# Optimization experiments

Hardware: AMD Instinct MI355X
Metric: run time of the kernel (lower is better)

Reference implementation:

```python
import jax, jax.numpy as jnp
import numpy as np

C1, C2, C3, S = 3, 6, 3, 16
SPLITS = (9 * C1 * 1, C1, 9 * C2 * C1, C2, 9 * C3 * C2, C3, 9 * S * C3, S)  # sums to 811
B = 16384


def _channelize(w, cin, cout):
    # w: [B, cout*9*cin] -> filter [3, 3, cin, B*cout] (B-major on out axis)
    w = w.reshape(-1, cout, 9 * cin)
    w = jnp.transpose(w, (2, 0, 1))          # [9*cin, B, cout]
    return w.reshape(3, 3, cin, -1)


def _gconv(x, w, groups):
    # x: [1, H, W, B*cin], w: [3, 3, cin, B*cout]; grouped conv, groups=B
    return jax.lax.conv_general_dilated(
        x, w, window_strides=(1, 1), padding='VALID',
        dimension_numbers=('NHWC', 'HWIO', 'NHWC'),
        feature_group_count=groups)


def _maxpool2(x):
    return jax.lax.reduce_window(x, -jnp.inf, jax.lax.max,
                                 (1, 2, 2, 1), (1, 2, 2, 1), 'VALID')


def setup_inputs() -> dict:
    key = jax.random.key(0)
    ks = jax.random.split(key, 8)
    tot = sum(SPLITS)
    return {
        'image': jax.random.normal(ks[0], (1, 28, 28, B), jnp.float32),
        'state': jax.random.normal(ks[1], (B, S), jnp.float32),
        'W1': jax.random.normal(ks[2], (S, 16), jnp.float32) * 0.25,
        'b1': jnp.zeros((16,), jnp.float32),
        'W2': jax.random.normal(ks[3], (16, 16), jnp.float32) * 0.25,
        'b2': jnp.zeros((16,), jnp.float32),
        'W3': jax.random.normal(ks[4], (16, tot), jnp.float32) * 0.1,
        'b3': jnp.zeros((tot,), jnp.float32),
    }


def reference(image, state, W1, b1, W2, b2, W3, b3):
    batch = state.shape[0]
    # Hypernetwork MLP producing per-sample conv weights (dropout rate 0 => identity)
    h = jax.nn.relu(state @ W1 + b1)
    h = jax.nn.relu(h @ W2 + b2)
    w = h @ W3 + b3                               # [B, 811]
    idx = np.cumsum(SPLITS)[:-1]
    w1, bb1, w2, bb2, w3, bb3, w4, bb4 = jnp.split(w, idx, axis=1)

    x = _gconv(image, _channelize(w1, 1, C1), batch) + bb1.reshape(-1)   # [1,26,26,B*C1]
    x = _maxpool2(jax.nn.relu(x))                                        # [1,13,13,B*C1]
    x = _gconv(x, _channelize(w2, C1, C2), batch) + bb2.reshape(-1)      # [1,11,11,B*C2]
    x = _maxpool2(jax.nn.relu(x))                                        # [1,5,5,B*C2]
    x = _gconv(x, _channelize(w3, C2, C3), batch) + bb3.reshape(-1)      # [1,3,3,B*C3]
    x = jax.nn.relu(x)
    x = _gconv(x, _channelize(w4, C3, S), batch) + bb4.reshape(-1)       # [1,1,1,B*S]
    x = jnp.transpose(x, (3, 1, 2, 0)).reshape(-1, S)                    # [B, S]
    return state + x
```

## Files before the change

### kernel.cpp

```cpp
#include <hip/hip_runtime.h>

#define BLK   512
#define NSAMP 8
#define REG   1480
#define OFF_P2   0
#define OFF_P3   152
#define OFF_W    392
#define HW_P1    2408
#define DW_P1    1204


typedef short bf16x8 __attribute__((ext_vector_type(8)));
typedef float f32x4  __attribute__((ext_vector_type(4)));
typedef float f32x2  __attribute__((ext_vector_type(2)));


__device__ __forceinline__ float bf2f(unsigned short u) {
    return __uint_as_float(((unsigned int)u) << 16);
}
__device__ __forceinline__ unsigned short f2bf(float f) {
    unsigned int x = __float_as_uint(f);
    return (unsigned short)((x + 0x7fffu + ((x >> 16) & 1u)) >> 16);
}
__device__ __forceinline__ void wsync() {
    __builtin_amdgcn_wave_barrier();
    __asm__ volatile("s_waitcnt lgkmcnt(0)" ::: "memory");
    __builtin_amdgcn_wave_barrier();
}

__device__ __forceinline__ bool is_bf16(const void* p, int elems) {
    const unsigned short* h = (const unsigned short*)p;
    int n = elems; if (n > 32) n = 32;
    int nz = 0, ok = 0;
    for (int i = 0; i < n; i += 2) {
        unsigned short u = h[i];
        if (u == 0) continue;
        ++nz;
        unsigned int e = (u >> 7) & 255u;
        if (e >= 100u && e <= 141u) ++ok;
    }
    if (nz < 4) return true;
    return 4 * ok >= 3 * nz;
}

__device__ __forceinline__ int wperm(int j) {
    if (j >= 30 && j < 192) {
        int rel = j - 30, c = rel / 27, r2 = rel - 27 * c;
        int tap = r2 / 3, ci = r2 - 3 * tap;
        return 30 + c * 27 + ci * 9 + tap;
    }
    if (j >= 198 && j < 360) {
        int rel = j - 198, c = rel / 54, r3 = rel - 54 * c;
        int tap = r3 / 6, ci = r3 - 6 * tap;
        return 198 + c * 54 + ci * 9 + tap;
    }
    return j;
}

__global__ __launch_bounds__(BLK, 4)
void dyncnn4_kernel(const void* __restrict__ image,
                    const void* __restrict__ state,
                    const void* __restrict__ W1, const void* __restrict__ b1,
                    const void* __restrict__ W2, const void* __restrict__ b2,
                    const void* __restrict__ W3, const void* __restrict__ b3,
                    void* __restrict__ out,
                    int B, int nswz)
{
    __shared__ float SH[NSAMP * REG];
    __shared__ float s_st[NSAMP][16];
    __shared__ float s_h1[NSAMP][16];
    __shared__ float s_h2[NSAMP][16];
    __shared__ unsigned char s_fl[8];
    __shared__ unsigned short s_pj[812];

    const int t    = threadIdx.x;
    const int wv   = t >> 6;
    const int lane = t & 63;
    const int hn   = lane & 15;
    const int kg   = lane >> 4;

    if (t < 8) {
        const void* q; int n;
        switch (t) {
            case 0:  q = image; n = 784 * B; break;
            case 1:  q = state; n = 16 * B;  break;
            case 2:  q = W1;    n = 256;     break;
            case 3:  q = b1;    n = 16;      break;
            case 4:  q = W2;    n = 256;     break;
            case 5:  q = b2;    n = 16;      break;
            case 6:  q = W3;    n = 12976;   break;
            default: q = b3;    n = 811;     break;
        }
        s_fl[t] = is_bf16(q, n) ? 1 : 0;
    }
    for (int j = t; j < 811; j += BLK)
        s_pj[j] = (unsigned short)wperm(j);
    __syncthreads();
    const bool im_bf = s_fl[0], st_bf = s_fl[1], w1_bf = s_fl[2], b1_bf = s_fl[3];
    const bool w2_bf = s_fl[4], b2_bf = s_fl[5], w3_bf = s_fl[6], b3_bf = s_fl[7];
    const bool out_bf = im_bf && st_bf && w1_bf && w2_bf && w3_bf;

    int p = blockIdx.x;
    int l = (nswz > 0) ? ((p & 7) * nswz + (p >> 3)) : p;
    const int b0 = l * NSAMP;

    unsigned short* su = (unsigned short*)SH;

    bf16x8 bp0 = {0,0,0,0,0,0,0,0}, bp1 = {0,0,0,0,0,0,0,0}, bp2 = {0,0,0,0,0,0,0,0},
           bp3 = {0,0,0,0,0,0,0,0}, bp4 = {0,0,0,0,0,0,0,0}, bp5 = {0,0,0,0,0,0,0,0},
           bp6 = {0,0,0,0,0,0,0,0};
    if (w3_bf) {
        const unsigned short* W3h = (const unsigned short*)W3;
#define PREF(T, BP) { const int tl = wv + (T) * 8; const int jn = tl * 16 + hn;      \
        if (kg < 2 && tl < 51 && jn < 811) {                                          \
            const unsigned short* q = W3h + (kg * 8) * 811 + jn;                      \
            BP[0] = (short)q[0];      BP[1] = (short)q[811];                          \
            BP[2] = (short)q[1622];   BP[3] = (short)q[2433];                         \
            BP[4] = (short)q[3244];   BP[5] = (short)q[4055];                         \
            BP[6] = (short)q[4866];   BP[7] = (short)q[5677]; } }
        PREF(0, bp0) PREF(1, bp1) PREF(2, bp2) PREF(3, bp3)
        PREF(4, bp4) PREF(5, bp5) PREF(6, bp6)
#undef PREF
    }

    if (wv < 2) {
        int s = wv * 4 + (lane >> 4), j = lane & 15;
        int gi = (b0 + s) * 16 + j;
        s_st[s][j] = st_bf ? bf2f(((const unsigned short*)state)[gi])
                           : ((const float*)state)[gi];
        wsync();
        float acc = b1_bf ? bf2f(((const unsigned short*)b1)[j])
                          : ((const float*)b1)[j];
#pragma unroll
        for (int k = 0; k < 16; ++k) {
            float w = w1_bf ? bf2f(((const unsigned short*)W1)[k * 16 + j])
                            : ((const float*)W1)[k * 16 + j];
            acc += s_st[s][k] * w;
        }
        s_h1[s][j] = fmaxf(acc, 0.f);
        wsync();
        acc = b2_bf ? bf2f(((const unsigned short*)b2)[j])
                    : ((const float*)b2)[j];
#pragma unroll
        for (int k = 0; k < 16; ++k) {
            float w = w2_bf ? bf2f(((const unsigned short*)W2)[k * 16 + j])
                            : ((const float*)W2)[k * 16 + j];
            acc += s_h1[s][k] * w;
        }
        s_h2[s][j] = fmaxf(acc, 0.f);
    } else {
        if (im_bf) {
            const unsigned short* im = (const unsigned short*)image;
            unsigned* sd = (unsigned*)SH;
            int d = t - 128;
            {
                const uint4 v0 = *(const uint4*)(im + (2 * d)     * B + b0);
                const uint4 v1 = *(const uint4*)(im + (2 * d + 1) * B + b0);
                unsigned a0[4] = {v0.x, v0.y, v0.z, v0.w};
                unsigned a1[4] = {v1.x, v1.y, v1.z, v1.w};
#pragma unroll
                for (int s = 0; s < 8; ++s) {
                    unsigned m = __builtin_amdgcn_perm(
                        a1[s >> 1], a0[s >> 1],
                        (s & 1) ? 0x07060302u : 0x05040100u);
                    sd[s * REG + d] = m;
                }
            }
            if (d < 8) {
                const int d2 = d + 384;
                const uint4 v0 = *(const uint4*)(im + (2 * d2)     * B + b0);
                const uint4 v1 = *(const uint4*)(im + (2 * d2 + 1) * B + b0);
                unsigned a0[4] = {v0.x, v0.y, v0.z, v0.w};
                unsigned a1[4] = {v1.x, v1.y, v1.z, v1.w};
#pragma unroll
                for (int s = 0; s < 8; ++s) {
                    unsigned m = __builtin_amdgcn_perm(
                        a1[s >> 1], a0[s >> 1],
                        (s & 1) ? 0x07060302u : 0x05040100u);
                    sd[s * REG + d2] = m;
                }
            }
        } else {
            const float* im = (const float*)image;
            int pix0 = t - 128;
            for (int pix = pix0; pix < 784; pix += 384) {
                const float4 a = *(const float4*)(im + pix * B + b0);
                const float4 c = *(const float4*)(im + pix * B + b0 + 4);
                su[0 * 2 * REG + pix] = f2bf(a.x);
                su[1 * 2 * REG + pix] = f2bf(a.y);
                su[2 * 2 * REG + pix] = f2bf(a.z);
                su[3 * 2 * REG + pix] = f2bf(a.w);
                su[4 * 2 * REG + pix] = f2bf(c.x);
                su[5 * 2 * REG + pix] = f2bf(c.y);
                su[6 * 2 * REG + pix] = f2bf(c.z);
                su[7 * 2 * REG + pix] = f2bf(c.w);
            }
        }
    }
    __syncthreads();

    {
        bf16x8 afrag;
#pragma unroll
        for (int i = 0; i < 8; ++i) afrag[i] = 0;
        if (kg < 2 && hn < 8) {
            const int k0 = kg * 8;
#pragma unroll
            for (int i = 0; i < 8; ++i)
                afrag[i] = (short)f2bf(s_h2[hn][k0 + i]);
        }
        const unsigned short* b3h = (const unsigned short*)b3;
        const float*          b3f = (const float*)b3;
        if (w3_bf) {
#define HTILE(T, BP) { const int tl = wv + (T) * 8; const int jn = tl * 16 + hn;     \
            f32x4 c = {0.f, 0.f, 0.f, 0.f};                                           \
            c = __builtin_amdgcn_mfma_f32_16x16x32_bf16(afrag, BP, c, 0, 0, 0);       \
            const int row0 = kg * 4;                                                  \
            if (tl < 51 && row0 < 8 && jn < 811) {                                    \
                float bb = b3_bf ? bf2f(b3h[jn]) : b3f[jn];                            \
                const int pj = (int)s_pj[jn];                                         \
                SH[(row0 + 0) * REG + OFF_W + pj] = c[0] + bb;                        \
                SH[(row0 + 1) * REG + OFF_W + pj] = c[1] + bb;                        \
                SH[(row0 + 2) * REG + OFF_W + pj] = c[2] + bb;                        \
                SH[(row0 + 3) * REG + OFF_W + pj] = c[3] + bb; } }
            HTILE(0, bp0) HTILE(1, bp1) HTILE(2, bp2) HTILE(3, bp3)
            HTILE(4, bp4) HTILE(5, bp5) HTILE(6, bp6)
#undef HTILE
        } else {
            for (int tile = wv; tile < 51; tile += 8) {
                const int jn = tile * 16 + hn;
                bf16x8 bfrag;
#pragma unroll
                for (int i = 0; i < 8; ++i) bfrag[i] = 0;
                if (kg < 2 && jn < 811) {
                    const int k0 = kg * 8;
                    const float* q = (const float*)W3 + k0 * 811 + jn;
#pragma unroll
                    for (int i = 0; i < 8; ++i) bfrag[i] = (short)f2bf(q[i * 811]);
                }
                f32x4 c = {0.f, 0.f, 0.f, 0.f};
                c = __builtin_amdgcn_mfma_f32_16x16x32_bf16(afrag, bfrag, c, 0, 0, 0);
                const int row0 = kg * 4;
                if (row0 < 8 && jn < 811) {
                    float bb = b3_bf ? bf2f(b3h[jn]) : b3f[jn];
                    const int pj = (int)s_pj[jn];
#pragma unroll
                    for (int r = 0; r < 4; ++r)
                        SH[(row0 + r) * REG + OFF_W + pj] = c[r] + bb;
                }
            }
        }
    }
    __syncthreads();

    const int sb  = wv * REG;
    const int sb2 = wv * 2 * REG;

    {
        float wc[27], cb[3];
#pragma unroll
        for (int i = 0; i < 27; ++i) wc[i] = SH[sb + OFF_W + i];
#pragma unroll
        for (int c = 0; c < 3; ++c) cb[c] = SH[sb + OFF_W + 27 + c];
        const unsigned* suw = (const unsigned*)&SH[sb];
#pragma unroll
        for (int it = 0; it < 3; ++it) {
            int pix = lane + it * 64;
            if (pix < 169) {
                int py = pix / 13, px = pix - py * 13;
                int iy = 2 * py;
                f32x2 P[4][3];
#pragma unroll
                for (int dy = 0; dy < 4; ++dy) {
                    int r = (iy + dy) * 14 + px;
                    unsigned d0 = suw[r], d1 = suw[r + 1];
                    float c0 = __uint_as_float(d0 << 16);
                    float c1 = __uint_as_float(d0 & 0xffff0000u);
                    float c2 = __uint_as_float(d1 << 16);
                    float c3 = __uint_as_float(d1 & 0xffff0000u);
                    P[dy][0] = (f32x2){c0, c1};
                    P[dy][1] = (f32x2){c1, c2};
                    P[dy][2] = (f32x2){c2, c3};
                }
                unsigned short* op = &su[sb2 + HW_P1 + py * 14 + px];
#pragma unroll
                for (int c = 0; c < 3; ++c) {
                    f32x2 at = {0.f, 0.f}, ab = {0.f, 0.f};
#pragma unroll
                    for (int ky = 0; ky < 3; ++ky)
#pragma unroll
                        for (int kx = 0; kx < 3; ++kx) {
                            float w = wc[c * 9 + ky * 3 + kx];
                            f32x2 ws = {w, w};
                            at += P[ky][kx]     * ws;
                            ab += P[ky + 1][kx] * ws;
                        }
                    float m = fmaxf(fmaxf(at.x, at.y), fmaxf(ab.x, ab.y));
                    op[c * 182] = f2bf(fmaxf(m + cb[c], 0.f));
                }
            }
        }
    }
    wsync();

    {
        int g = lane >> 5, q = lane & 31;
        if (q < 25) {
            int py = q / 5, px = q - py * 5;
            const unsigned* p1w = (const unsigned*)&SH[sb + DW_P1];
            f32x2 aT0 = {0.f, 0.f}, aB0 = {0.f, 0.f};
            f32x2 aT1 = {0.f, 0.f}, aB1 = {0.f, 0.f};
            f32x2 aT2 = {0.f, 0.f}, aB2 = {0.f, 0.f};
#pragma unroll
            for (int ci = 0; ci < 3; ++ci) {
                f32x2 P[4][3];
#pragma unroll
                for (int dy = 0; dy < 4; ++dy) {
                    int r = ci * 91 + (2 * py + dy) * 7 + px;
                    unsigned d0 = p1w[r], d1 = p1w[r + 1];
                    float c0 = __uint_as_float(d0 << 16);
                    float c1 = __uint_as_float(d0 & 0xffff0000u);
                    float c2 = __uint_as_float(d1 << 16);
                    float c3 = __uint_as_float(d1 & 0xffff0000u);
                    P[dy][0] = (f32x2){c0, c1};
                    P[dy][1] = (f32x2){c1, c2};
                    P[dy][2] = (f32x2){c2, c3};
                }
#pragma unroll
                for (int it = 0; it < 3; ++it) {
                    int c = it * 2 + g;
                    const int wo = sb + OFF_W + 30 + c * 27 + ci * 9;
#pragma unroll
                    for (int ky = 0; ky < 3; ++ky)
#pragma unroll
                        for (int kx = 0; kx < 3; ++kx) {
                            float w = SH[wo + ky * 3 + kx];
                            f32x2 ws = {w, w};
                            if (it == 0) { aT0 += P[ky][kx] * ws; aB0 += P[ky + 1][kx] * ws; }
                            if (it == 1) { aT1 += P[ky][kx] * ws; aB1 += P[ky + 1][kx] * ws; }
                            if (it == 2) { aT2 += P[ky][kx] * ws; aB2 += P[ky + 1][kx] * ws; }
                        }
                }
            }
#pragma unroll
            for (int it = 0; it < 3; ++it) {
                int c = it * 2 + g;
                f32x2 aT = (it == 0) ? aT0 : (it == 1) ? aT1 : aT2;
                f32x2 aB = (it == 0) ? aB0 : (it == 1) ? aB1 : aB2;
                float m = fmaxf(fmaxf(aT.x, aT.y), fmaxf(aB.x, aB.y));
                SH[sb + OFF_P2 + c * 25 + q] =
                    fmaxf(m + SH[sb + OFF_W + 192 + c], 0.f);
            }
        }
    }
    wsync();

    {
        float acc = 0.f;
        int pq = lane % 27;
        int half = lane / 27;
        int c = pq / 9, pos = pq - c * 9;
        int py = pos / 3, px = pos - py * 3;
        if (lane < 54) {
            const int cb3 = half * 3;
#pragma unroll
            for (int ci3 = 0; ci3 < 3; ++ci3) {
                const int ci = cb3 + ci3;
                const int wo = sb + OFF_W + 198 + c * 54 + ci * 9;
                float wr[9];
#pragma unroll
                for (int i = 0; i < 9; ++i) wr[i] = SH[wo + i];
                const int pbase = sb + OFF_P2 + ci * 25 + py * 5 + px;
#pragma unroll
                for (int ky = 0; ky < 3; ++ky)
#pragma unroll
                    for (int kx = 0; kx < 3; ++kx)
                        acc += SH[pbase + ky * 5 + kx] * wr[ky * 3 + kx];
            }
        }
        float other = __shfl(acc, (lane + 27) & 63);
        if (lane < 27)
            SH[sb + OFF_P3 + pos * 3 + c] =
                fmaxf(acc + other + SH[sb + OFF_W + 360 + c], 0.f);
    }
    wsync();

    {
        float acc = 0.f;
        int os = lane & 15, h = (lane >> 4) & 1;
        if (lane < 32) {
            const int wo = sb + OFF_W + 363 + os * 27;
            int p0 = h ? 4 : 0, p1 = h ? 9 : 4;
            for (int pp = p0; pp < p1; ++pp)
#pragma unroll
                for (int ci = 0; ci < 3; ++ci)
                    acc += SH[sb + OFF_P3 + pp * 3 + ci] * SH[wo + pp * 3 + ci];
        }
        float other = __shfl(acc, (lane + 16) & 63);
        if (lane < 16) {
            float tot = acc + other + SH[sb + OFF_W + 795 + os] + s_st[wv][os];
            int gi = (b0 + wv) * 16 + os;
            if (out_bf) ((unsigned short*)out)[gi] = f2bf(tot);
            else        ((float*)out)[gi] = tot;
        }
    }
}

extern "C" void kernel_launch(void* const* d_in, const int* in_sizes, int n_in,
                              void* d_out, int out_size, void* d_ws, size_t ws_size,
                              hipStream_t stream) {
    (void)d_ws; (void)ws_size; (void)n_in; (void)out_size;
    int B = in_sizes[1] / 16;
    int nblocks = B / NSAMP;
    int nswz = (nblocks % 8 == 0) ? (nblocks / 8) : 0;

    dyncnn4_kernel<<<nblocks, BLK, 0, stream>>>(
        d_in[0], d_in[1], d_in[2], d_in[3], d_in[4], d_in[5], d_in[6], d_in[7],
        d_out, B, nswz);
}
```

Before: 138.8 us.

## Convert to persistent grid with software-pipelined staging of next sample group

Replaces the one-block-per-8-samples launch with a persistent grid of at most 768 blocks that loop over sample groups. After conv1 of the current group, it loads the next group's image and runs its MLP while conv2–conv4 of the current group proceed. The p2/p3 intermediates move into the upper part of the per-sample region so they do not collide with the freshly staged image, and the state buffer is double-buffered. The cost is extra block-wide barriers per iteration and loss of the W3 register prefetch, since W3 is now reloaded per group. The per-wave conv1 reads of the current image versus other waves' writes of the next image may also need checking.

```diff
diff --git a/kernel.cpp b/kernel.cpp
--- a/kernel.cpp
+++ b/kernel.cpp
@@ -3,12 +3,12 @@
 #define BLK   512
 #define NSAMP 8
 #define REG   1480
-#define OFF_P2   0
-#define OFF_P3   152
+#define GRID  768
 #define OFF_W    392
 #define HW_P1    2408
 #define DW_P1    1204
-
+#define DW_P2    1204
+#define DW_P3    1364
 
 typedef short bf16x8 __attribute__((ext_vector_type(8)));
 typedef float f32x4  __attribute__((ext_vector_type(4)));
@@ -57,6 +57,141 @@
     return j;
 }
 
+
+__device__ __forceinline__ void do_stage(const void* image, float* SH, int B,
+                                         int b0, int t, bool im_bf)
+{
+    unsigned short* su = (unsigned short*)SH;
+    if (im_bf) {
+        const unsigned short* im = (const unsigned short*)image;
+        unsigned* sd = (unsigned*)SH;
+        int d = t - 128;
+        {
+            const uint4 v0 = *(const uint4*)(im + (2 * d)     * B + b0);
+            const uint4 v1 = *(const uint4*)(im + (2 * d + 1) * B + b0);
+            unsigned a0[4] = {v0.x, v0.y, v0.z, v0.w};
+            unsigned a1[4] = {v1.x, v1.y, v1.z, v1.w};
+#pragma unroll
+            for (int s = 0; s < 8; ++s) {
+                unsigned m = __builtin_amdgcn_perm(
+                    a1[s >> 1], a0[s >> 1],
+                    (s & 1) ? 0x07060302u : 0x05040100u);
+                sd[s * REG + d] = m;
+            }
+        }
+        if (d < 8) {
+            const int d2 = d + 384;
+            const uint4 v0 = *(const uint4*)(im + (2 * d2)     * B + b0);
+            const uint4 v1 = *(const uint4*)(im + (2 * d2 + 1) * B + b0);
+            unsigned a0[4] = {v0.x, v0.y, v0.z, v0.w};
+            unsigned a1[4] = {v1.x, v1.y, v1.z, v1.w};
+#pragma unroll
+            for (int s = 0; s < 8; ++s) {
+                unsigned m = __builtin_amdgcn_perm(
+                    a1[s >> 1], a0[s >> 1],
+                    (s & 1) ? 0x07060302u : 0x05040100u);
+                sd[s * REG + d2] = m;
+            }
+        }
+    } else {
+        const float* im = (const float*)image;
+        int pix0 = t - 128;
+        for (int pix = pix0; pix < 784; pix += 384) {
+            const float4 a = *(const float4*)(im + pix * B + b0);
+            const float4 c = *(const float4*)(im + pix * B + b0 + 4);
+            su[0 * 2 * REG + pix] = f2bf(a.x);
+            su[1 * 2 * REG + pix] = f2bf(a.y);
+            su[2 * 2 * REG + pix] = f2bf(a.z);
+            su[3 * 2 * REG + pix] = f2bf(a.w);
+            su[4 * 2 * REG + pix] = f2bf(c.x);
+            su[5 * 2 * REG + pix] = f2bf(c.y);
+            su[6 * 2 * REG + pix] = f2bf(c.z);
+            su[7 * 2 * REG + pix] = f2bf(c.w);
+        }
+    }
+}
+
+__device__ __forceinline__ void do_mlp(const void* state,
+                                       const void* W1, const void* b1,
+                                       const void* W2, const void* b2,
+                                       float (*st)[16], float (*h1)[16], float (*h2)[16],
+                                       int b0, int wv, int lane,
+                                       bool st_bf, bool w1_bf, bool b1_bf,
+                                       bool w2_bf, bool b2_bf)
+{
+    int s = wv * 4 + (lane >> 4), j = lane & 15;
+    int gi = (b0 + s) * 16 + j;
+    st[s][j] = st_bf ? bf2f(((const unsigned short*)state)[gi])
+                     : ((const float*)state)[gi];
+    wsync();
+    float acc = b1_bf ? bf2f(((const unsigned short*)b1)[j])
+                      : ((const float*)b1)[j];
+#pragma unroll
+    for (int k = 0; k < 16; ++k) {
+        float w = w1_bf ? bf2f(((const unsigned short*)W1)[k * 16 + j])
+                        : ((const float*)W1)[k * 16 + j];
+        acc += st[s][k] * w;
+    }
+    h1[s][j] = fmaxf(acc, 0.f);
+    wsync();
+    acc = b2_bf ? bf2f(((const unsigned short*)b2)[j])
+                : ((const float*)b2)[j];
+#pragma unroll
+    for (int k = 0; k < 16; ++k) {
+        float w = w2_bf ? bf2f(((const unsigned short*)W2)[k * 16 + j])
+                        : ((const float*)W2)[k * 16 + j];
+        acc += h1[s][k] * w;
+    }
+    h2[s][j] = fmaxf(acc, 0.f);
+}
+
+__device__ __forceinline__ void do_head(const void* W3, const void* b3,
+                                        float* SH, float (*h2)[16],
+                                        const unsigned short* s_pj,
+                                        int wv, int hn, int kg,
+                                        bool w3_bf, bool b3_bf)
+{
+    bf16x8 afrag;
+#pragma unroll
+    for (int i = 0; i < 8; ++i) afrag[i] = 0;
+    if (kg < 2 && hn < 8) {
+        const int k0 = kg * 8;
+#pragma unroll
+        for (int i = 0; i < 8; ++i)
+            afrag[i] = (short)f2bf(h2[hn][k0 + i]);
+    }
+    const unsigned short* b3h = (const unsigned short*)b3;
+    const float*          b3f = (const float*)b3;
+    for (int tile = wv; tile < 51; tile += 8) {
+        const int jn = tile * 16 + hn;
+        bf16x8 bfrag;
+#pragma unroll
+        for (int i = 0; i < 8; ++i) bfrag[i] = 0;
+        if (kg < 2 && jn < 811) {
+            const int k0 = kg * 8;
+            if (w3_bf) {
+                const unsigned short* q = (const unsigned short*)W3 + k0 * 811 + jn;
+#pragma unroll
+                for (int i = 0; i < 8; ++i) bfrag[i] = (short)q[i * 811];
+            } else {
+                const float* q = (const float*)W3 + k0 * 811 + jn;
+#pragma unroll
+                for (int i = 0; i < 8; ++i) bfrag[i] = (short)f2bf(q[i * 811]);
+            }
+        }
+        f32x4 c = {0.f, 0.f, 0.f, 0.f};
+        c = __builtin_amdgcn_mfma_f32_16x16x32_bf16(afrag, bfrag, c, 0, 0, 0);
+        const int row0 = kg * 4;
+        if (row0 < 8 && jn < 811) {
+            float bb = b3_bf ? bf2f(b3h[jn]) : b3f[jn];
+            const int pj = (int)s_pj[jn];
+#pragma unroll
+            for (int r = 0; r < 4; ++r)
+                SH[(row0 + r) * REG + OFF_W + pj] = c[r] + bb;
+        }
+    }
+}
+
 __global__ __launch_bounds__(BLK, 4)
 void dyncnn4_kernel(const void* __restrict__ image,
                     const void* __restrict__ state,
@@ -64,10 +199,10 @@
                     const void* __restrict__ W2, const void* __restrict__ b2,
                     const void* __restrict__ W3, const void* __restrict__ b3,
                     void* __restrict__ out,
-                    int B, int nswz)
+                    int B, int ngrp, int nswz)
 {
     __shared__ float SH[NSAMP * REG];
-    __shared__ float s_st[NSAMP][16];
+    __shared__ float s_st[2][NSAMP][16];
     __shared__ float s_h1[NSAMP][16];
     __shared__ float s_h2[NSAMP][16];
     __shared__ unsigned char s_fl[8];
@@ -100,309 +235,193 @@
     const bool w2_bf = s_fl[4], b2_bf = s_fl[5], w3_bf = s_fl[6], b3_bf = s_fl[7];
     const bool out_bf = im_bf && st_bf && w1_bf && w2_bf && w3_bf;
 
-    int p = blockIdx.x;
-    int l = (nswz > 0) ? ((p & 7) * nswz + (p >> 3)) : p;
-    const int b0 = l * NSAMP;
+    int g = blockIdx.x;
+    if (g >= ngrp) return;
+    const int stride = gridDim.x;
+
+    int lg = (nswz > 0) ? ((g & 7) * nswz + (g >> 3)) : g;
+    int b0 = lg * NSAMP;
 
     unsigned short* su = (unsigned short*)SH;
 
-    bf16x8 bp0 = {0,0,0,0,0,0,0,0}, bp1 = {0,0,0,0,0,0,0,0}, bp2 = {0,0,0,0,0,0,0,0},
-           bp3 = {0,0,0,0,0,0,0,0}, bp4 = {0,0,0,0,0,0,0,0}, bp5 = {0,0,0,0,0,0,0,0},
-           bp6 = {0,0,0,0,0,0,0,0};
-    if (w3_bf) {
-        const unsigned short* W3h = (const unsigned short*)W3;
-#define PREF(T, BP) { const int tl = wv + (T) * 8; const int jn = tl * 16 + hn;      \
-        if (kg < 2 && tl < 51 && jn < 811) {                                          \
-            const unsigned short* q = W3h + (kg * 8) * 811 + jn;                      \
-            BP[0] = (short)q[0];      BP[1] = (short)q[811];                          \
-            BP[2] = (short)q[1622];   BP[3] = (short)q[2433];                         \
-            BP[4] = (short)q[3244];   BP[5] = (short)q[4055];                         \
-            BP[6] = (short)q[4866];   BP[7] = (short)q[5677]; } }
-        PREF(0, bp0) PREF(1, bp1) PREF(2, bp2) PREF(3, bp3)
-        PREF(4, bp4) PREF(5, bp5) PREF(6, bp6)
-#undef PREF
-    }
-
-    if (wv < 2) {
-        int s = wv * 4 + (lane >> 4), j = lane & 15;
-        int gi = (b0 + s) * 16 + j;
-        s_st[s][j] = st_bf ? bf2f(((const unsigned short*)state)[gi])
-                           : ((const float*)state)[gi];
+    if (wv < 2) do_mlp(state, W1, b1, W2, b2, s_st[0], s_h1, s_h2, b0, wv, lane,
+                       st_bf, w1_bf, b1_bf, w2_bf, b2_bf);
+    else        do_stage(image, SH, B, b0, t, im_bf);
+    __syncthreads();
+    do_head(W3, b3, SH, s_h2, s_pj, wv, hn, kg, w3_bf, b3_bf);
+    __syncthreads();
+
+    int buf = 0;
+    for (;;) {
+        const int sb  = wv * REG;
+        const int sb2 = wv * 2 * REG;
+
+        {
+            float wc[27], cb[3];
+#pragma unroll
+            for (int i = 0; i < 27; ++i) wc[i] = SH[sb + OFF_W + i];
+#pragma unroll
+            for (int c = 0; c < 3; ++c) cb[c] = SH[sb + OFF_W + 27 + c];
+            const unsigned* suw = (const unsigned*)&SH[sb];
+#pragma unroll
+            for (int it = 0; it < 3; ++it) {
+                int pix = lane + it * 64;
+                if (pix < 169) {
+                    int py = pix / 13, px = pix - py * 13;
+                    int iy = 2 * py;
+                    f32x2 P[4][3];
+#pragma unroll
+                    for (int dy = 0; dy < 4; ++dy) {
+                        int r = (iy + dy) * 14 + px;
+                        unsigned d0 = suw[r], d1 = suw[r + 1];
+                        float c0 = __uint_as_float(d0 << 16);
+                        float c1 = __uint_as_float(d0 & 0xffff0000u);
+                        float c2 = __uint_as_float(d1 << 16);
+                        float c3 = __uint_as_float(d1 & 0xffff0000u);
+                        P[dy][0] = (f32x2){c0, c1};
+                        P[dy][1] = (f32x2){c1, c2};
+                        P[dy][2] = (f32x2){c2, c3};
+                    }
+                    unsigned short* op = &su[sb2 + HW_P1 + py * 14 + px];
+#pragma unroll
+                    for (int c = 0; c < 3; ++c) {
+                        f32x2 at = {0.f, 0.f}, ab = {0.f, 0.f};
+#pragma unroll
+                        for (int ky = 0; ky < 3; ++ky)
+#pragma unroll
+                            for (int kx = 0; kx < 3; ++kx) {
+                                float w = wc[c * 9 + ky * 3 + kx];
+                                f32x2 ws = {w, w};
+                                at += P[ky][kx]     * ws;
+                                ab += P[ky + 1][kx] * ws;
+                            }
+                        float m = fmaxf(fmaxf(at.x, at.y), fmaxf(ab.x, ab.y));
+                        op[c * 182] = f2bf(fmaxf(m + cb[c], 0.f));
+                    }
+                }
+            }
+        }
+        __syncthreads();
+
+        int gn = g + stride;
+        bool more = (gn < ngrp);
+        int b0n = 0;
+        if (more) {
+            int lgn = (nswz > 0) ? ((gn & 7) * nswz + (gn >> 3)) : gn;
+            b0n = lgn * NSAMP;
+            if (wv < 2) do_mlp(state, W1, b1, W2, b2, s_st[buf ^ 1], s_h1, s_h2,
+                               b0n, wv, lane, st_bf, w1_bf, b1_bf, w2_bf, b2_bf);
+            else        do_stage(image, SH, B, b0n, t, im_bf);
+        }
+
+        {
+            int gq = lane >> 5, q = lane & 31;
+            if (q < 25) {
+                int py = q / 5, px = q - py * 5;
+                const unsigned* p1w = (const unsigned*)&SH[sb + DW_P1];
+                f32x2 aT0 = {0.f,0.f}, aB0 = {0.f,0.f};
+                f32x2 aT1 = {0.f,0.f}, aB1 = {0.f,0.f};
+                f32x2 aT2 = {0.f,0.f}, aB2 = {0.f,0.f};
+#pragma unroll
+                for (int ci = 0; ci < 3; ++ci) {
+                    f32x2 P[4][3];
+#pragma unroll
+                    for (int dy = 0; dy < 4; ++dy) {
+                        int r = ci * 91 + (2 * py + dy) * 7 + px;
+                        unsigned d0 = p1w[r], d1 = p1w[r + 1];
+                        float c0 = __uint_as_float(d0 << 16);
+                        float c1 = __uint_as_float(d0 & 0xffff0000u);
+                        float c2 = __uint_as_float(d1 << 16);
+                        float c3 = __uint_as_float(d1 & 0xffff0000u);
+                        P[dy][0] = (f32x2){c0, c1};
+                        P[dy][1] = (f32x2){c1, c2};
+                        P[dy][2] = (f32x2){c2, c3};
+                    }
+#pragma unroll
+                    for (int it = 0; it < 3; ++it) {
+                        int c = it * 2 + gq;
+                        const int wo = sb + OFF_W + 30 + c * 27 + ci * 9;
+#pragma unroll
+                        for (int ky = 0; ky < 3; ++ky)
+#pragma unroll
+                            for (int kx = 0; kx < 3; ++kx) {
+                                float w = SH[wo + ky * 3 + kx];
+                                f32x2 ws = {w, w};
+                                if (it == 0) { aT0 += P[ky][kx] * ws; aB0 += P[ky+1][kx] * ws; }
+                                if (it == 1) { aT1 += P[ky][kx] * ws; aB1 += P[ky+1][kx] * ws; }
+                                if (it == 2) { aT2 += P[ky][kx] * ws; aB2 += P[ky+1][kx] * ws; }
+                            }
+                    }
+                }
+#pragma unroll
+                for (int it = 0; it < 3; ++it) {
+                    int c = it * 2 + gq;
+                    f32x2 aT = (it == 0) ? aT0 : (it == 1) ? aT1 : aT2;
+                    f32x2 aB = (it == 0) ? aB0 : (it == 1) ? aB1 : aB2;
+                    float m = fmaxf(fmaxf(aT.x, aT.y), fmaxf(aB.x, aB.y));
+                    SH[sb + DW_P2 + c * 25 + q] =
+                        fmaxf(m + SH[sb + OFF_W + 192 + c], 0.f);
+                }
+            }
+        }
         wsync();
-        float acc = b1_bf ? bf2f(((const unsigned short*)b1)[j])
-                          : ((const float*)b1)[j];
-#pragma unroll
-        for (int k = 0; k < 16; ++k) {
-            float w = w1_bf ? bf2f(((const unsigned short*)W1)[k * 16 + j])
-                            : ((const float*)W1)[k * 16 + j];
-            acc += s_st[s][k] * w;
-        }
-        s_h1[s][j] = fmaxf(acc, 0.f);
+
+        {
+            float acc = 0.f;
+            int pq = lane % 27;
+            int half = lane / 27;
+            int c = pq / 9, pos = pq - c * 9;
+            int py = pos / 3, px = pos - py * 3;
+            if (lane < 54) {
+                const int cb3 = half * 3;
+#pragma unroll
+                for (int ci3 = 0; ci3 < 3; ++ci3) {
+                    const int ci = cb3 + ci3;
+                    const int wo = sb + OFF_W + 198 + c * 54 + ci * 9;
+                    float wr[9];
+#pragma unroll
+                    for (int i = 0; i < 9; ++i) wr[i] = SH[wo + i];
+                    const int pbase = sb + DW_P2 + ci * 25 + py * 5 + px;
+#pragma unroll
+                    for (int ky = 0; ky < 3; ++ky)
+#pragma unroll
+                        for (int kx = 0; kx < 3; ++kx)
+                            acc += SH[pbase + ky * 5 + kx] * wr[ky * 3 + kx];
+                }
+            }
+            float other = __shfl(acc, (lane + 27) & 63);
+            if (lane < 27)
+                SH[sb + DW_P3 + pos * 3 + c] =
+                    fmaxf(acc + other + SH[sb + OFF_W + 360 + c], 0.f);
+        }
         wsync();
-        acc = b2_bf ? bf2f(((const unsigned short*)b2)[j])
-                    : ((const float*)b2)[j];
-#pragma unroll
-        for (int k = 0; k < 16; ++k) {
-            float w = w2_bf ? bf2f(((const unsigned short*)W2)[k * 16 + j])
-                            : ((const float*)W2)[k * 16 + j];
-            acc += s_h1[s][k] * w;
-        }
-        s_h2[s][j] = fmaxf(acc, 0.f);
-    } else {
-        if (im_bf) {
-            const unsigned short* im = (const unsigned short*)image;
-            unsigned* sd = (unsigned*)SH;
-            int d = t - 128;
-            {
-                const uint4 v0 = *(const uint4*)(im + (2 * d)     * B + b0);
-                const uint4 v1 = *(const uint4*)(im + (2 * d + 1) * B + b0);
-                unsigned a0[4] = {v0.x, v0.y, v0.z, v0.w};
-                unsigned a1[4] = {v1.x, v1.y, v1.z, v1.w};
-#pragma unroll
-                for (int s = 0; s < 8; ++s) {
-                    unsigned m = __builtin_amdgcn_perm(
-                        a1[s >> 1], a0[s >> 1],
-                        (s & 1) ? 0x07060302u : 0x05040100u);
-                    sd[s * REG + d] = m;
-                }
-            }
-            if (d < 8) {
-                const int d2 = d + 384;
-                const uint4 v0 = *(const uint4*)(im + (2 * d2)     * B + b0);
-                const uint4 v1 = *(const uint4*)(im + (2 * d2 + 1) * B + b0);
-                unsigned a0[4] = {v0.x, v0.y, v0.z, v0.w};
-                unsigned a1[4] = {v1.x, v1.y, v1.z, v1.w};
-#pragma unroll
-                for (int s = 0; s < 8; ++s) {
-                    unsigned m = __builtin_amdgcn_perm(
-                        a1[s >> 1], a0[s >> 1],
-                        (s & 1) ? 0x07060302u : 0x05040100u);
-                    sd[s * REG + d2] = m;
-                }
-            }
-        } else {
-            const float* im = (const float*)image;
-            int pix0 = t - 128;
-            for (int pix = pix0; pix < 784; pix += 384) {
-                const float4 a = *(const float4*)(im + pix * B + b0);
-                const float4 c = *(const float4*)(im + pix * B + b0 + 4);
-                su[0 * 2 * REG + pix] = f2bf(a.x);
-                su[1 * 2 * REG + pix] = f2bf(a.y);
-                su[2 * 2 * REG + pix] = f2bf(a.z);
-                su[3 * 2 * REG + pix] = f2bf(a.w);
-                su[4 * 2 * REG + pix] = f2bf(c.x);
-                su[5 * 2 * REG + pix] = f2bf(c.y);
-                su[6 * 2 * REG + pix] = f2bf(c.z);
-                su[7 * 2 * REG + pix] = f2bf(c.w);
-            }
-        }
-    }
-    __syncthreads();
-
-    {
-        bf16x8 afrag;
-#pragma unroll
-        for (int i = 0; i < 8; ++i) afrag[i] = 0;
-        if (kg < 2 && hn < 8) {
-            const int k0 = kg * 8;
-#pragma unroll
-            for (int i = 0; i < 8; ++i)
-                afrag[i] = (short)f2bf(s_h2[hn][k0 + i]);
-        }
-        const unsigned short* b3h = (const unsigned short*)b3;
-        const float*          b3f = (const float*)b3;
-        if (w3_bf) {
-#define HTILE(T, BP) { const int tl = wv + (T) * 8; const int jn = tl * 16 + hn;     \
-            f32x4 c = {0.f, 0.f, 0.f, 0.f};                                           \
-            c = __builtin_amdgcn_mfma_f32_16x16x32_bf16(afrag, BP, c, 0, 0, 0);       \
-            const int row0 = kg * 4;                                                  \
-            if (tl < 51 && row0 < 8 && jn < 811) {                                    \
-                float bb = b3_bf ? bf2f(b3h[jn]) : b3f[jn];                            \
-                const int pj = (int)s_pj[jn];                                         \
-                SH[(row0 + 0) * REG + OFF_W + pj] = c[0] + bb;                        \
-                SH[(row0 + 1) * REG + OFF_W + pj] = c[1] + bb;                        \
-                SH[(row0 + 2) * REG + OFF_W + pj] = c[2] + bb;                        \
-                SH[(row0 + 3) * REG + OFF_W + pj] = c[3] + bb; } }
-            HTILE(0, bp0) HTILE(1, bp1) HTILE(2, bp2) HTILE(3, bp3)
-            HTILE(4, bp4) HTILE(5, bp5) HTILE(6, bp6)
-#undef HTILE
-        } else {
-            for (int tile = wv; tile < 51; tile += 8) {
-                const int jn = tile * 16 + hn;
-                bf16x8 bfrag;
-#pragma unroll
-                for (int i = 0; i < 8; ++i) bfrag[i] = 0;
-                if (kg < 2 && jn < 811) {
-                    const int k0 = kg * 8;
-                    const float* q = (const float*)W3 + k0 * 811 + jn;
-#pragma unroll
-                    for (int i = 0; i < 8; ++i) bfrag[i] = (short)f2bf(q[i * 811]);
-                }
-                f32x4 c = {0.f, 0.f, 0.f, 0.f};
-                c = __builtin_amdgcn_mfma_f32_16x16x32_bf16(afrag, bfrag, c, 0, 0, 0);
-                const int row0 = kg * 4;
-                if (row0 < 8 && jn < 811) {
-                    float bb = b3_bf ? bf2f(b3h[jn]) : b3f[jn];
-                    const int pj = (int)s_pj[jn];
-#pragma unroll
-                    for (int r = 0; r < 4; ++r)
-                        SH[(row0 + r) * REG + OFF_W + pj] = c[r] + bb;
-                }
-            }
-        }
-    }
-    __syncthreads();
-
-    const int sb  = wv * REG;
-    const int sb2 = wv * 2 * REG;
-
-    {
-        float wc[27], cb[3];
-#pragma unroll
-        for (int i = 0; i < 27; ++i) wc[i] = SH[sb + OFF_W + i];
-#pragma unroll
-        for (int c = 0; c < 3; ++c) cb[c] = SH[sb + OFF_W + 27 + c];
-        const unsigned* suw = (const unsigned*)&SH[sb];
-#pragma unroll
-        for (int it = 0; it < 3; ++it) {
-            int pix = lane + it * 64;
-            if (pix < 169) {
-                int py = pix / 13, px = pix - py * 13;
-                int iy = 2 * py;
-                f32x2 P[4][3];
-#pragma unroll
-                for (int dy = 0; dy < 4; ++dy) {
-                    int r = (iy + dy) * 14 + px;
-                    unsigned d0 = suw[r], d1 = suw[r + 1];
-                    float c0 = __uint_as_float(d0 << 16);
-                    float c1 = __uint_as_float(d0 & 0xffff0000u);
-                    float c2 = __uint_as_float(d1 << 16);
-                    float c3 = __uint_as_float(d1 & 0xffff0000u);
-                    P[dy][0] = (f32x2){c0, c1};
-                    P[dy][1] = (f32x2){c1, c2};
-                    P[dy][2] = (f32x2){c2, c3};
-                }
-                unsigned short* op = &su[sb2 + HW_P1 + py * 14 + px];
-#pragma unroll
-                for (int c = 0; c < 3; ++c) {
-                    f32x2 at = {0.f, 0.f}, ab = {0.f, 0.f};
-#pragma unroll
-                    for (int ky = 0; ky < 3; ++ky)
-#pragma unroll
-                        for (int kx = 0; kx < 3; ++kx) {
-                            float w = wc[c * 9 + ky * 3 + kx];
-                            f32x2 ws = {w, w};
-                            at += P[ky][kx]     * ws;
-                            ab += P[ky + 1][kx] * ws;
-                        }
-                    float m = fmaxf(fmaxf(at.x, at.y), fmaxf(ab.x, ab.y));
-                    op[c * 182] = f2bf(fmaxf(m + cb[c], 0.f));
-                }
-            }
-        }
-    }
-    wsync();
-
-    {
-        int g = lane >> 5, q = lane & 31;
-        if (q < 25) {
-            int py = q / 5, px = q - py * 5;
-            const unsigned* p1w = (const unsigned*)&SH[sb + DW_P1];
-            f32x2 aT0 = {0.f, 0.f}, aB0 = {0.f, 0.f};
-            f32x2 aT1 = {0.f, 0.f}, aB1 = {0.f, 0.f};
-            f32x2 aT2 = {0.f, 0.f}, aB2 = {0.f, 0.f};
-#pragma unroll
-            for (int ci = 0; ci < 3; ++ci) {
-                f32x2 P[4][3];
-#pragma unroll
-                for (int dy = 0; dy < 4; ++dy) {
-                    int r = ci * 91 + (2 * py + dy) * 7 + px;
-                    unsigned d0 = p1w[r], d1 = p1w[r + 1];
-                    float c0 = __uint_as_float(d0 << 16);
-                    float c1 = __uint_as_float(d0 & 0xffff0000u);
-                    float c2 = __uint_as_float(d1 << 16);
-                    float c3 = __uint_as_float(d1 & 0xffff0000u);
-                    P[dy][0] = (f32x2){c0, c1};
-                    P[dy][1] = (f32x2){c1, c2};
-                    P[dy][2] = (f32x2){c2, c3};
-                }
-#pragma unroll
-                for (int it = 0; it < 3; ++it) {
-                    int c = it * 2 + g;
-                    const int wo = sb + OFF_W + 30 + c * 27 + ci * 9;
-#pragma unroll
-                    for (int ky = 0; ky < 3; ++ky)
-#pragma unroll
-                        for (int kx = 0; kx < 3; ++kx) {
-                            float w = SH[wo + ky * 3 + kx];
-                            f32x2 ws = {w, w};
-                            if (it == 0) { aT0 += P[ky][kx] * ws; aB0 += P[ky + 1][kx] * ws; }
-                            if (it == 1) { aT1 += P[ky][kx] * ws; aB1 += P[ky + 1][kx] * ws; }
-                            if (it == 2) { aT2 += P[ky][kx] * ws; aB2 += P[ky + 1][kx] * ws; }
-                        }
-                }
-            }
-#pragma unroll
-            for (int it = 0; it < 3; ++it) {
-                int c = it * 2 + g;
-                f32x2 aT = (it == 0) ? aT0 : (it == 1) ? aT1 : aT2;
-                f32x2 aB = (it == 0) ? aB0 : (it == 1) ? aB1 : aB2;
-                float m = fmaxf(fmaxf(aT.x, aT.y), fmaxf(aB.x, aB.y));
-                SH[sb + OFF_P2 + c * 25 + q] =
-                    fmaxf(m + SH[sb + OFF_W + 192 + c], 0.f);
-            }
-        }
-    }
-    wsync();
-
-    {
-        float acc = 0.f;
-        int pq = lane % 27;
-        int half = lane / 27;
-        int c = pq / 9, pos = pq - c * 9;
-        int py = pos / 3, px = pos - py * 3;
-        if (lane < 54) {
-            const int cb3 = half * 3;
-#pragma unroll
-            for (int ci3 = 0; ci3 < 3; ++ci3) {
-                const int ci = cb3 + ci3;
-                const int wo = sb + OFF_W + 198 + c * 54 + ci * 9;
-                float wr[9];
-#pragma unroll
-                for (int i = 0; i < 9; ++i) wr[i] = SH[wo + i];
-                const int pbase = sb + OFF_P2 + ci * 25 + py * 5 + px;
-#pragma unroll
-                for (int ky = 0; ky < 3; ++ky)
-#pragma unroll
-                    for (int kx = 0; kx < 3; ++kx)
-                        acc += SH[pbase + ky * 5 + kx] * wr[ky * 3 + kx];
-            }
-        }
-        float other = __shfl(acc, (lane + 27) & 63);
-        if (lane < 27)
-            SH[sb + OFF_P3 + pos * 3 + c] =
-                fmaxf(acc + other + SH[sb + OFF_W + 360 + c], 0.f);
-    }
-    wsync();
-
-    {
-        float acc = 0.f;
-        int os = lane & 15, h = (lane >> 4) & 1;
-        if (lane < 32) {
-            const int wo = sb + OFF_W + 363 + os * 27;
-            int p0 = h ? 4 : 0, p1 = h ? 9 : 4;
-            for (int pp = p0; pp < p1; ++pp)
-#pragma unroll
-                for (int ci = 0; ci < 3; ++ci)
-                    acc += SH[sb + OFF_P3 + pp * 3 + ci] * SH[wo + pp * 3 + ci];
-        }
-        float other = __shfl(acc, (lane + 16) & 63);
-        if (lane < 16) {
-            float tot = acc + other + SH[sb + OFF_W + 795 + os] + s_st[wv][os];
-            int gi = (b0 + wv) * 16 + os;
-            if (out_bf) ((unsigned short*)out)[gi] = f2bf(tot);
-            else        ((float*)out)[gi] = tot;
-        }
+
+        {
+            float acc = 0.f;
+            int os = lane & 15, h = (lane >> 4) & 1;
+            if (lane < 32) {
+                const int wo = sb + OFF_W + 363 + os * 27;
+                int p0 = h ? 4 : 0, p1 = h ? 9 : 4;
+                for (int pp = p0; pp < p1; ++pp)
+#pragma unroll
+                    for (int ci = 0; ci < 3; ++ci)
+                        acc += SH[sb + DW_P3 + pp * 3 + ci] * SH[wo + pp * 3 + ci];
+            }
+            float other = __shfl(acc, (lane + 16) & 63);
+            if (lane < 16) {
+                float tot = acc + other + SH[sb + OFF_W + 795 + os]
+                          + s_st[buf][wv][os];
+                int gi = (b0 + wv) * 16 + os;
+                if (out_bf) ((unsigned short*)out)[gi] = f2bf(tot);
+                else        ((float*)out)[gi] = tot;
+            }
+        }
+        __syncthreads();
+
+        if (!more) break;
+        do_head(W3, b3, SH, s_h2, s_pj, wv, hn, kg, w3_bf, b3_bf);
+        __syncthreads();
+        g = gn; b0 = b0n; buf ^= 1;
     }
 }
 
@@ -411,10 +430,11 @@
                               hipStream_t stream) {
     (void)d_ws; (void)ws_size; (void)n_in; (void)out_size;
     int B = in_sizes[1] / 16;
-    int nblocks = B / NSAMP;
-    int nswz = (nblocks % 8 == 0) ? (nblocks / 8) : 0;
-
-    dyncnn4_kernel<<<nblocks, BLK, 0, stream>>>(
+    int ngrp = B / NSAMP;
+    int nswz = (ngrp % 8 == 0) ? (ngrp / 8) : 0;
+    int grid = (ngrp < GRID) ? ngrp : GRID;
+
+    dyncnn4_kernel<<<grid, BLK, 0, stream>>>(
         d_in[0], d_in[1], d_in[2], d_in[3], d_in[4], d_in[5], d_in[6], d_in[7],
-        d_out, B, nswz);
-}
+        d_out, B, ngrp, nswz);
+}
```

Result: slower. 184.6 us (+33.0%).
